# Kernel optimization log

Hardware: AMD Instinct MI355X
Metric: run time of the kernel (lower is better)

The kernel has to match this reference:

```python
import jax, jax.numpy as jnp
import numpy as np

N_NODES = 100000
IN_CH = 128
HID_CH = 128
N_EDGES = 1600000


def setup_inputs() -> dict:
    key = jax.random.key(0)
    ks = jax.random.split(key, 8)
    x = jax.random.normal(ks[0], (N_NODES, IN_CH), dtype=jnp.float32)
    edge_index = jax.random.randint(ks[1], (2, N_EDGES), 0, N_NODES, dtype=jnp.int64)
    s1 = 1.0 / np.sqrt(IN_CH)
    s2 = 1.0 / np.sqrt(HID_CH)
    # SAGEConv layer 1: lin_l (aggregated neighbors, has bias), lin_r (root)
    Wl1 = jax.random.uniform(ks[2], (IN_CH, HID_CH), jnp.float32, -s1, s1)
    Wr1 = jax.random.uniform(ks[3], (IN_CH, HID_CH), jnp.float32, -s1, s1)
    b1 = jnp.zeros((HID_CH,), jnp.float32)
    # SAGEConv layer 2
    Wl2 = jax.random.uniform(ks[4], (HID_CH, HID_CH), jnp.float32, -s2, s2)
    Wr2 = jax.random.uniform(ks[5], (HID_CH, HID_CH), jnp.float32, -s2, s2)
    b2 = jnp.zeros((HID_CH,), jnp.float32)
    return {"x": x, "edge_index": edge_index,
            "Wl1": Wl1, "Wr1": Wr1, "b1": b1,
            "Wl2": Wl2, "Wr2": Wr2, "b2": b2}


def _sage_conv(x, src, dst, inv_deg, Wl, Wr, b):
    # mean aggregation of source-node features into destination nodes
    agg = jax.ops.segment_sum(x[src], dst, num_segments=N_NODES)  # [N, d]
    mean = agg * inv_deg[:, None]
    # out = lin_l(mean_neighbors) + lin_r(x)
    return mean @ Wl + x @ Wr + b


def reference(x, edge_index, Wl1, Wr1, b1, Wl2, Wr2, b2):
    src = edge_index[0]
    dst = edge_index[1]
    deg = jax.ops.segment_sum(jnp.ones_like(dst, dtype=jnp.float32), dst,
                              num_segments=N_NODES)
    inv_deg = 1.0 / jnp.maximum(deg, 1.0)
    h = jax.nn.relu(_sage_conv(x, src, dst, inv_deg, Wl1, Wr1, b1))
    # F.dropout(p=0.2, training=False) is identity in eval mode
    h = jax.nn.relu(_sage_conv(h, src, dst, inv_deg, Wl2, Wr2, b2))
    return h
```

## Files before the change

kernel.cpp:

```cpp
#include <hip/hip_runtime.h>

#define NN 100000
#define NE 1600000
#define CH 128

#define PART 512
#define NP 196
#define PCAP 8704
#define NB 391
#define SCAP 64
#define SLAB 1536

typedef __attribute__((ext_vector_type(8))) short bf16x8;
typedef __attribute__((ext_vector_type(4))) float f32x4;
typedef unsigned int uint;
typedef unsigned short ushort;

__device__ __forceinline__ ushort f2b(float f) {
    uint u = __builtin_bit_cast(uint, f);
    uint r = (u + 0x7fff + ((u >> 16) & 1)) >> 16;
    return (ushort)r;
}
__device__ __forceinline__ float blo(uint v) { return __builtin_bit_cast(float, v << 16); }
__device__ __forceinline__ float bhi(uint v) { return __builtin_bit_cast(float, v & 0xffff0000u); }

__device__ __forceinline__ void acc8(float* a, uint4 v) {
    a[0] += blo(v.x); a[1] += bhi(v.x);
    a[2] += blo(v.y); a[3] += bhi(v.y);
    a[4] += blo(v.z); a[5] += bhi(v.z);
    a[6] += blo(v.w); a[7] += bhi(v.w);
}


__global__ __launch_bounds__(1024) void k_bin(const int4* __restrict__ src4, const int4* __restrict__ dst4,
                                              uint* __restrict__ pcnt, uint* __restrict__ pairbuf) {
    __shared__ uint slots[NP * SCAP];
    __shared__ uint lcnt[NP];
    __shared__ uint lbase[NP];
    int tid = threadIdx.x;
    if (tid < NP) lcnt[tid] = 0;
    __syncthreads();
    int e4 = blockIdx.x * 1024 + tid;
    if (e4 < NE / 4) {
        int4 d4 = dst4[e4];
        int4 s4 = src4[e4];
        int dd[4] = {d4.x, d4.y, d4.z, d4.w};
        int ss[4] = {s4.x, s4.y, s4.z, s4.w};
        #pragma unroll
        for (int j = 0; j < 4; ++j) {
            int p = dd[j] >> 9;
            uint pair = ((uint)(dd[j] & 511) << 17) | (uint)ss[j];
            uint pos = atomicAdd(&lcnt[p], 1u);
            if (pos < SCAP) slots[p * SCAP + pos] = pair;
        }
    }
    __syncthreads();
    if (tid < NP) {
        uint c = lcnt[tid];
        c = c < SCAP ? c : SCAP;
        lcnt[tid] = c;
        lbase[tid] = atomicAdd(&pcnt[tid], c);
    }
    __syncthreads();
    for (int t = tid; t < NP * SCAP; t += 1024) {
        int p = t >> 6;
        uint s = (uint)(t & (SCAP - 1));
        if (s < lcnt[p]) {
            uint idx = lbase[p] + s;
            if (idx < PCAP) pairbuf[(size_t)p * PCAP + idx] = slots[t];
        }
    }
}


__global__ __launch_bounds__(512) void k_mid(const uint* __restrict__ pcnt, const uint* __restrict__ pairbuf,
                                             int* __restrict__ nbrG, uint* __restrict__ pack,
                                             const float* __restrict__ x, ushort* __restrict__ xb,
                                             const float* __restrict__ Wl1, const float* __restrict__ Wr1,
                                             const float* __restrict__ Wl2, const float* __restrict__ Wr2,
                                             ushort* __restrict__ BtK1, ushort* __restrict__ BtK2) {
    __shared__ uint pairs[PCAP];
    __shared__ uint cnt[PART];
    __shared__ uint rowptr[PART + 1];
    __shared__ uint wpart[8];
    int tid = threadIdx.x;
    int b = blockIdx.x;
    if (b >= NP) {
        int i = b - NP;
        if (i < 784) {
            int p = i / 196;
            int n = (i % 196) * 512 + tid;
            if (n >= NN) return;
            const float4* sp = (const float4*)(x + (size_t)n * 128 + p * 32);
            uint4 o[4];
            ushort* op = (ushort*)o;
            #pragma unroll
            for (int q = 0; q < 8; ++q) {
                float4 v = sp[q];
                op[q * 4 + 0] = f2b(v.x);
                op[q * 4 + 1] = f2b(v.y);
                op[q * 4 + 2] = f2b(v.z);
                op[q * 4 + 3] = f2b(v.w);
            }
            uint4* dp = (uint4*)(xb + ((size_t)p * NN + n) * 32);
            #pragma unroll
            for (int q = 0; q < 4; ++q) dp[q] = o[q];
        } else {
            int idx = (i - 784) * 512 + tid;
            int L = idx >> 15;
            int ii = idx & 32767;
            const float* Wl = L ? Wl2 : Wl1;
            const float* Wr = L ? Wr2 : Wr1;
            ushort* BtK = L ? BtK2 : BtK1;
            int c = ii & 31;
            int n = (ii >> 5) & 127;
            int kt = ii >> 12;
            int k = kt * 32 + c;
            float v = (k < 128) ? Wl[k * 128 + n] : Wr[(k - 128) * 128 + n];
            BtK[ii] = f2b(v);
        }
        return;
    }
    int p = b;
    uint tot = pcnt[p];
    tot = tot < PCAP ? tot : PCAP;
    for (uint i = tid; i < tot; i += 512) pairs[i] = pairbuf[(size_t)p * PCAP + i];
    cnt[tid] = 0;
    __syncthreads();
    for (uint i = tid; i < tot; i += 512) atomicAdd(&cnt[pairs[i] >> 17], 1u);
    __syncthreads();
    uint deg = cnt[tid];
    uint s = deg;
    #pragma unroll
    for (int off = 1; off < 64; off <<= 1) {
        uint t = __shfl_up(s, off, 64);
        if ((tid & 63) >= off) s += t;
    }
    if ((tid & 63) == 63) wpart[tid >> 6] = s;
    __syncthreads();
    uint base = 0;
    int w = tid >> 6;
    #pragma unroll
    for (int q = 0; q < 7; ++q) base += (q < w) ? wpart[q] : 0;
    rowptr[tid] = base + s - deg;
    if (tid == 511) rowptr[512] = base + s;
    cnt[tid] = 0;
    __syncthreads();
    for (uint i = tid; i < tot; i += 512) {
        uint u = pairs[i];
        uint dl = u >> 17;
        uint pos = rowptr[dl] + atomicAdd(&cnt[dl], 1u);
        nbrG[(size_t)p * PCAP + pos] = (int)(u & 0x1FFFFu);
    }
    {
        int n = p * PART + tid;
        if (n < NN) {
            uint d = rowptr[tid + 1] - rowptr[tid];
            pack[n] = ((uint)(p * PCAP) + rowptr[tid]) | (d << 21);
        }
    }
}


__global__ __launch_bounds__(256) void k_agg(const uint4* __restrict__ feat, const int* __restrict__ nbrG,
                                             const uint* __restrict__ pack, uint4* __restrict__ outb) {
    __shared__ int sl[SLAB];
    __shared__ int sh_s0, sh_cnt;
    int plane = blockIdx.x;
    int nb = blockIdx.y * 64;
    int tid = threadIdx.x;
    int n = nb + (tid >> 2);
    int h = tid & 3;
    if (tid == 0) {
        uint u0 = pack[nb];
        int last = nb + 63 < NN ? nb + 63 : NN - 1;
        uint u1 = pack[last];
        int s0 = (int)(u0 & 0x1FFFFFu);
        sh_s0 = s0;
        sh_cnt = (int)(u1 & 0x1FFFFFu) + (int)(u1 >> 21) - s0;
    }
    __syncthreads();
    int s0 = sh_s0, scnt = sh_cnt;
    bool staged = scnt <= SLAB;
    if (staged) {
        for (int i = tid; i < scnt; i += 256) sl[i] = nbrG[s0 + i];
    }
    __syncthreads();
    if (n >= NN) return;
    uint u = pack[n];
    int s = (int)(u & 0x1FFFFFu);
    int d = (int)(u >> 21);
    const char* fb = (const char*)feat + ((size_t)plane * NN) * 64;
    uint hoff = (uint)h * 16;
    float a[8] = {};
    if (staged) {
        const int* bp = sl + (s - s0);
        int i = 0;
        for (; i + 8 <= d; i += 8) {
            uint off[8];
            uint4 v[8];
            #pragma unroll
            for (int j = 0; j < 8; ++j) off[j] = ((uint)bp[i + j] << 6) | hoff;
            #pragma unroll
            for (int j = 0; j < 8; ++j) v[j] = *(const uint4*)(fb + off[j]);
            #pragma unroll
            for (int j = 0; j < 8; ++j) acc8(a, v[j]);
        }
        for (; i < d; ++i) acc8(a, *(const uint4*)(fb + (((uint)bp[i] << 6) | hoff)));
    } else {
        const int* bp = nbrG + s;
        int i = 0;
        for (; i + 4 <= d; i += 4) {
            uint o0 = ((uint)bp[i] << 6) | hoff;
            uint o1 = ((uint)bp[i + 1] << 6) | hoff;
            uint o2 = ((uint)bp[i + 2] << 6) | hoff;
            uint o3 = ((uint)bp[i + 3] << 6) | hoff;
            uint4 v0 = *(const uint4*)(fb + o0);
            uint4 v1 = *(const uint4*)(fb + o1);
            uint4 v2 = *(const uint4*)(fb + o2);
            uint4 v3 = *(const uint4*)(fb + o3);
            acc8(a, v0);
            acc8(a, v1);
            acc8(a, v2);
            acc8(a, v3);
        }
        for (; i < d; ++i) acc8(a, *(const uint4*)(fb + (((uint)bp[i] << 6) | hoff)));
    }
    float id = 1.0f / fmaxf((float)d, 1.0f);
    uint4 r;
    r.x = (uint)f2b(a[0] * id) | ((uint)f2b(a[1] * id) << 16);
    r.y = (uint)f2b(a[2] * id) | ((uint)f2b(a[3] * id) << 16);
    r.z = (uint)f2b(a[4] * id) | ((uint)f2b(a[5] * id) << 16);
    r.w = (uint)f2b(a[6] * id) | ((uint)f2b(a[7] * id) << 16);
    outb[((size_t)plane * NN + n) * 4 + h] = r;
}


template <bool WB16>
__global__ __launch_bounds__(256) void k_gemm(const ushort* __restrict__ Am, const ushort* Ax,
                                              const ushort* __restrict__ BtK, const float* __restrict__ bias,
                                              void* outp, int M) {
    int lane = threadIdx.x & 63;
    int wave = threadIdx.x >> 6;
    int bm = blockIdx.x * 128 + wave * 32;
    int l16 = lane & 15;
    int lk8 = (lane >> 4) * 8;

    f32x4 acc[2][8] = {};
    #pragma unroll
    for (int kt = 0; kt < 8; ++kt) {
        const ushort* A = (kt < 4) ? Am : Ax;
        int p = kt & 3;
        bf16x8 af[2];
        #pragma unroll
        for (int mt = 0; mt < 2; ++mt) {
            int row = bm + mt * 16 + l16;
            row = row < M ? row : M - 1;
            af[mt] = *(const bf16x8*)(A + ((size_t)p * NN + row) * 32 + lk8);
        }
        const ushort* Bk = BtK + (size_t)kt * 128 * 32;
        #pragma unroll
        for (int nt = 0; nt < 8; ++nt) {
            bf16x8 bfr = *(const bf16x8*)(Bk + (size_t)(nt * 16 + l16) * 32 + lk8);
            acc[0][nt] = __builtin_amdgcn_mfma_f32_16x16x32_bf16(af[0], bfr, acc[0][nt], 0, 0, 0);
            acc[1][nt] = __builtin_amdgcn_mfma_f32_16x16x32_bf16(af[1], bfr, acc[1][nt], 0, 0, 0);
        }
    }
    int mr0 = (lane >> 4) * 4;
    #pragma unroll
    for (int mt = 0; mt < 2; ++mt) {
        #pragma unroll
        for (int r = 0; r < 4; ++r) {
            int m = bm + mt * 16 + mr0 + r;
            if (m < M) {
                #pragma unroll
                for (int nt = 0; nt < 8; ++nt) {
                    float v = acc[mt][nt][r] + bias[nt * 16 + l16];
                    v = v > 0.f ? v : 0.f;
                    if (WB16) {
                        int ch = nt * 16 + l16;
                        ((ushort*)outp)[((size_t)(ch >> 5) * NN + m) * 32 + (ch & 31)] = f2b(v);
                    } else {
                        ((float*)outp)[(size_t)m * 128 + nt * 16 + l16] = v;
                    }
                }
            }
        }
    }
}


static inline size_t alignup(size_t x) { return (x + 255) & ~(size_t)255; }

extern "C" void kernel_launch(void* const* d_in, const int* in_sizes, int n_in,
                              void* d_out, int out_size, void* d_ws, size_t ws_size,
                              hipStream_t stream) {
    const float* x   = (const float*)d_in[0];
    const int* edge  = (const int*)d_in[1];
    const float* Wl1 = (const float*)d_in[2];
    const float* Wr1 = (const float*)d_in[3];
    const float* b1  = (const float*)d_in[4];
    const float* Wl2 = (const float*)d_in[5];
    const float* Wr2 = (const float*)d_in[6];
    const float* b2  = (const float*)d_in[7];
    float* out = (float*)d_out;

    const int* srcp = edge;
    const int* dstp = edge + NE;

    uint* pairbuf = (uint*)d_out;
    int* nbrG = (int*)d_out + (size_t)NP * PCAP;

    char* w = (char*)d_ws;
    uint* pcnt = (uint*)w;     w += alignup((size_t)NP * 4);
    uint* pack = (uint*)w;     w += alignup((size_t)NN * 4);
    ushort* xb = (ushort*)w;   w += alignup((size_t)NN * CH * 2);
    ushort* mb = (ushort*)w;   w += alignup((size_t)NN * CH * 2);
    ushort* BtK1 = (ushort*)w; w += alignup((size_t)128 * 256 * 2);
    ushort* BtK2 = (ushort*)w; w += alignup((size_t)128 * 256 * 2);

    hipMemsetAsync(pcnt, 0, (size_t)NP * 4, stream);

    k_bin<<<NB, 1024, 0, stream>>>((const int4*)srcp, (const int4*)dstp, pcnt, pairbuf);
    k_mid<<<NP + 784 + 128, 512, 0, stream>>>(pcnt, pairbuf, nbrG, pack,
                                              x, xb, Wl1, Wr1, Wl2, Wr2, BtK1, BtK2);

    int gg = (NN + 127) / 128;
    dim3 ag(4, (NN + 63) / 64);
    k_agg<<<ag, 256, 0, stream>>>((const uint4*)xb, nbrG, pack, (uint4*)mb);
    k_gemm<true><<<gg, 256, 0, stream>>>(mb, xb, BtK1, b1, (void*)xb, NN);
    k_agg<<<ag, 256, 0, stream>>>((const uint4*)xb, nbrG, pack, (uint4*)mb);
    k_gemm<false><<<gg, 256, 0, stream>>>(mb, xb, BtK2, b2, (void*)out, NN);
}
```

Before: 330.8 us.

## Stage GEMM weights in double-buffered swizzled LDS and coalesce bf16 output stores

The GEMM kernel now stages each K-slice of the transposed weight matrix into a double-buffered, XOR-swizzled LDS tile, and prefetches the next slice and the next A fragment from global memory while the MFMAs run on the current one. Tiles shrink to 64 rows per block (16 per wave), which doubles the grid. The bf16 epilogue goes through LDS so that each lane writes a 16-byte vector instead of scattered 2-byte stores. The aim is to cut redundant global weight loads and uncoalesced output writes, at the cost of a barrier per K step and less register-level reuse of B per wave.

```diff
diff --git a/kernel.cpp b/kernel.cpp
--- a/kernel.cpp
+++ b/kernel.cpp
@@ -240,49 +240,93 @@
 __global__ __launch_bounds__(256) void k_gemm(const ushort* __restrict__ Am, const ushort* Ax,
                                               const ushort* __restrict__ BtK, const float* __restrict__ bias,
                                               void* outp, int M) {
-    int lane = threadIdx.x & 63;
-    int wave = threadIdx.x >> 6;
-    int bm = blockIdx.x * 128 + wave * 32;
+    __shared__ char smem[17408];
+    int tid = threadIdx.x;
+    int lane = tid & 63;
+    int w = tid >> 6;
+    int bm = blockIdx.x * 64 + w * 16;
     int l16 = lane & 15;
-    int lk8 = (lane >> 4) * 8;
-
-    f32x4 acc[2][8] = {};
+    int g = lane >> 4;
+    int lk8 = g * 8;
+
+    int row = bm + l16;
+    row = row < M ? row : M - 1;
+
+    int uu0 = tid * 2;
+    uint sw = ((uint)(tid >> 1) & 7) << 4;
+    uint d0 = ((uint)uu0 * 16) ^ sw;
+    uint d1 = ((uint)(uu0 + 1) * 16) ^ sw;
+    uint rsw = ((uint)(l16 & 7)) << 4;
+
+    {
+        const uint4* gsrc = (const uint4*)BtK + uu0;
+        uint4 r0 = gsrc[0], r1 = gsrc[1];
+        *(uint4*)(smem + d0) = r0;
+        *(uint4*)(smem + d1) = r1;
+    }
+    const ushort* A0 = Am;
+    bf16x8 afc = *(const bf16x8*)(A0 + ((size_t)0 * NN + row) * 32 + lk8);
+    __syncthreads();
+
+    f32x4 acc[8] = {};
     #pragma unroll
     for (int kt = 0; kt < 8; ++kt) {
-        const ushort* A = (kt < 4) ? Am : Ax;
-        int p = kt & 3;
-        bf16x8 af[2];
-        #pragma unroll
-        for (int mt = 0; mt < 2; ++mt) {
-            int row = bm + mt * 16 + l16;
-            row = row < M ? row : M - 1;
-            af[mt] = *(const bf16x8*)(A + ((size_t)p * NN + row) * 32 + lk8);
-        }
-        const ushort* Bk = BtK + (size_t)kt * 128 * 32;
+        int cur = kt & 1;
+        uint4 r0, r1;
+        bf16x8 afn;
+        if (kt < 7) {
+            const uint4* gsrc = (const uint4*)(BtK + (size_t)(kt + 1) * 4096) + uu0;
+            r0 = gsrc[0];
+            r1 = gsrc[1];
+            const ushort* An = ((kt + 1) < 4) ? Am : Ax;
+            int pn = (kt + 1) & 3;
+            afn = *(const bf16x8*)(An + ((size_t)pn * NN + row) * 32 + lk8);
+        }
+        const char* bb = smem + cur * 8192;
         #pragma unroll
         for (int nt = 0; nt < 8; ++nt) {
-            bf16x8 bfr = *(const bf16x8*)(Bk + (size_t)(nt * 16 + l16) * 32 + lk8);
-            acc[0][nt] = __builtin_amdgcn_mfma_f32_16x16x32_bf16(af[0], bfr, acc[0][nt], 0, 0, 0);
-            acc[1][nt] = __builtin_amdgcn_mfma_f32_16x16x32_bf16(af[1], bfr, acc[1][nt], 0, 0, 0);
-        }
-    }
-    int mr0 = (lane >> 4) * 4;
-    #pragma unroll
-    for (int mt = 0; mt < 2; ++mt) {
+            uint off = (((uint)(nt * 16 + l16) * 64) + (uint)g * 16) ^ rsw;
+            bf16x8 bfr = *(const bf16x8*)(bb + off);
+            acc[nt] = __builtin_amdgcn_mfma_f32_16x16x32_bf16(afc, bfr, acc[nt], 0, 0, 0);
+        }
+        if (kt < 7) {
+            char* nb = smem + (cur ^ 1) * 8192;
+            *(uint4*)(nb + d0) = r0;
+            *(uint4*)(nb + d1) = r1;
+            afc = afn;
+        }
+        __syncthreads();
+    }
+
+    int mr0 = g * 4;
+    if (WB16) {
+        ushort (*so)[136] = (ushort(*)[136])(smem + w * 4352);
+        #pragma unroll
+        for (int r = 0; r < 4; ++r)
+            #pragma unroll
+            for (int nt = 0; nt < 8; ++nt) {
+                float v = acc[nt][r] + bias[nt * 16 + l16];
+                so[mr0 + r][nt * 16 + l16] = f2b(v > 0.f ? v : 0.f);
+            }
+        #pragma unroll
+        for (int pass = 0; pass < 4; ++pass) {
+            int u = pass * 64 + lane;
+            int rr = u >> 4, h16 = u & 15;
+            int m = blockIdx.x * 64 + w * 16 + rr;
+            if (m < M) {
+                bf16x8 vv = *(const bf16x8*)&so[rr][h16 * 8];
+                *(bf16x8*)((ushort*)outp + ((size_t)(h16 >> 2) * NN + m) * 32 + (h16 & 3) * 8) = vv;
+            }
+        }
+    } else {
         #pragma unroll
         for (int r = 0; r < 4; ++r) {
-            int m = bm + mt * 16 + mr0 + r;
+            int m = bm + mr0 + r;
             if (m < M) {
                 #pragma unroll
                 for (int nt = 0; nt < 8; ++nt) {
-                    float v = acc[mt][nt][r] + bias[nt * 16 + l16];
-                    v = v > 0.f ? v : 0.f;
-                    if (WB16) {
-                        int ch = nt * 16 + l16;
-                        ((ushort*)outp)[((size_t)(ch >> 5) * NN + m) * 32 + (ch & 31)] = f2b(v);
-                    } else {
-                        ((float*)outp)[(size_t)m * 128 + nt * 16 + l16] = v;
-                    }
+                    float v = acc[nt][r] + bias[nt * 16 + l16];
+                    ((float*)outp)[(size_t)m * 128 + nt * 16 + l16] = v > 0.f ? v : 0.f;
                 }
             }
         }
@@ -325,7 +369,7 @@
     k_mid<<<NP + 784 + 128, 512, 0, stream>>>(pcnt, pairbuf, nbrG, pack,
                                               x, xb, Wl1, Wr1, Wl2, Wr2, BtK1, BtK2);
 
-    int gg = (NN + 127) / 128;
+    int gg = (NN + 63) / 64;
     dim3 ag(4, (NN + 63) / 64);
     k_agg<<<ag, 256, 0, stream>>>((const uint4*)xb, nbrG, pack, (uint4*)mb);
     k_gemm<true><<<gg, 256, 0, stream>>>(mb, xb, BtK1, b1, (void*)xb, NN);
```

Result: faster. 296.0 us (-10.5%).
